# Performance work log

Hardware: AMD Instinct MI355X
Metric: run time of the kernel (lower is better)

Reference implementation:

```python
import jax, jax.numpy as jnp
import numpy as np

N, E = 50000, 400000
N_INP, H, D = 256, 4, 32
HID = H * D
TN, TE, L, N_OUT = 4, 6, 2, 16
SQRT_D = float(np.sqrt(D))


def setup_inputs() -> dict:
    key = jax.random.key(0)
    ks = jax.random.split(key, 16)
    s = 0.05
    return {
        "x": jax.random.normal(ks[0], (N, N_INP), jnp.float32),
        "adapt_W": jax.random.normal(ks[1], (TN, N_INP, HID), jnp.float32) * s,
        "adapt_b": jnp.zeros((TN, HID), jnp.float32),
        "Wk": jax.random.normal(ks[2], (L, TN, HID, HID), jnp.float32) * s,
        "Wq": jax.random.normal(ks[3], (L, TN, HID, HID), jnp.float32) * s,
        "Wv": jax.random.normal(ks[4], (L, TN, HID, HID), jnp.float32) * s,
        "pri": jnp.ones((L, H, TE), jnp.float32),
        "Wa": jax.random.normal(ks[5], (L, H, TE, D, D), jnp.float32) * s,
        "Wm": jax.random.normal(ks[6], (L, H, TE, D, D), jnp.float32) * s,
        "Wla": jax.random.normal(ks[7], (L, TN, HID, HID), jnp.float32) * s,
        "skip": jnp.ones((L, TN), jnp.float32),
        "gamma": jnp.ones((L, HID), jnp.float32),
        "beta": jnp.zeros((L, HID), jnp.float32),
        "out_W": jax.random.normal(ks[8], (HID, N_OUT), jnp.float32) * s,
        "out_b": jnp.zeros((N_OUT,), jnp.float32),
        "ntype": jax.random.randint(ks[9], (N,), 0, TN),
        "etype": jax.random.randint(ks[10], (E,), 0, TE),
        "src": jax.random.randint(ks[11], (E,), 0, N),
        "dst": jax.random.randint(ks[12], (E,), 0, N),
    }


def typed_linear(x, W, types):
    # out[i] = x[i] @ W[types[i]]  (TypedLinear / per-type nn.Linear loop)
    out = jnp.zeros((x.shape[0], W.shape[-1]), x.dtype)
    for t in range(W.shape[0]):
        out = jnp.where((types == t)[:, None], x @ W[t], out)
    return out


def hgt_layer(h, ntype, etype, src, dst, Wk, Wq, Wv, pri, Wa, Wm, Wla, skip, gamma, beta):
    k = typed_linear(h, Wk, ntype).reshape(N, H, D)
    q = typed_linear(h, Wq, ntype).reshape(N, H, D)
    v = typed_linear(h, Wv, ntype).reshape(N, H, D)
    k_e, q_e, v_e = k[src], q[dst], v[src]  # [E,H,D] gathers
    a = jnp.zeros((E, H), h.dtype)
    m = jnp.zeros((E, H, D), h.dtype)
    for t in range(TE):  # small fixed loop over edge types (relation matrices)
        sel = etype == t
        kw = jnp.einsum('ehd,hdo->eho', k_e, Wa[:, t])
        sc = (kw * q_e).sum(-1) * pri[:, t][None, :] / SQRT_D  # [E,H]
        a = jnp.where(sel[:, None], sc, a)
        mt = jnp.einsum('ehd,hdo->eho', v_e, Wm[:, t])
        m = jnp.where(sel[:, None, None], mt, m)
    # edge softmax over incoming edges of each destination node
    amax = jax.ops.segment_max(a, dst, num_segments=N)
    ex = jnp.exp(a - amax[dst])
    den = jax.ops.segment_sum(ex, dst, num_segments=N)
    attn = ex / den[dst]
    agg = jax.ops.segment_sum(m * attn[:, :, None], dst, num_segments=N).reshape(N, HID)
    ha = typed_linear(agg, Wla, ntype)
    alpha = jax.nn.sigmoid(skip)[ntype][:, None]
    out = ha * alpha + h * (1.0 - alpha)
    mu = out.mean(-1, keepdims=True)
    var = jnp.mean((out - mu) ** 2, -1, keepdims=True)
    return (out - mu) / jnp.sqrt(var + 1e-5) * gamma + beta


def forward(x, adapt_W, adapt_b, Wk, Wq, Wv, pri, Wa, Wm, Wla, skip, gamma, beta, out_W, out_b, ntype, etype, src, dst):
    # per-node-type adapt linear + exact GELU
    h = typed_linear(x, adapt_W, ntype) + adapt_b[ntype]
    h = jax.nn.gelu(h, approximate=False)
    for l in range(L):
        h = hgt_layer(h, ntype, etype, src, dst, Wk[l], Wq[l], Wv[l], pri[l], Wa[l], Wm[l], Wla[l], skip[l], gamma[l], beta[l])
    return h @ out_W + out_b


def reference(x, adapt_W, adapt_b, Wk, Wq, Wv, pri, Wa, Wm, Wla, skip, gamma, beta, out_W, out_b, ntype, etype, src, dst):
    return forward(x, adapt_W, adapt_b, Wk, Wq, Wv, pri, Wa, Wm, Wla, skip, gamma, beta, out_W, out_b, ntype, etype, src, dst)
```

## Files before the change

### kernel.cpp

```cpp
#include <hip/hip_runtime.h>
#include <hip/hip_bf16.h>
#include <math.h>

#define NN   50000
#define EE   400000
#define NINP 256
#define HH   4
#define DD   32
#define HIDD 128
#define TNN  4
#define TEE  6
#define LLL  2
#define NOUTT 16
#define NB   196


typedef __attribute__((ext_vector_type(8))) short bf16x8;
typedef __attribute__((ext_vector_type(4))) float f32x4;

__device__ __forceinline__ float bf_lo(unsigned u) { return __uint_as_float(u << 16); }
__device__ __forceinline__ float bf_hi(unsigned u) { return __uint_as_float(u & 0xFFFF0000u); }
__device__ __forceinline__ unsigned f2bf(float f) {
    unsigned u = __float_as_uint(f);
    u += 0x7FFFu + ((u >> 16) & 1u);
    return (u >> 16);
}

__global__ void k_init(int* __restrict__ deg, int* __restrict__ cur, int* __restrict__ ncnt,
                       int* __restrict__ ncur, int* __restrict__ nperm) {
    int i = blockIdx.x * 256 + threadIdx.x;
    if (i < NN) { deg[i] = 0; cur[i] = 0; }
    if (i < 16) { ncnt[i] = 0; ncur[i] = 0; }
    if (i < NN + 512) nperm[i] = -1;
}

__global__ void k_count_edges(const int* __restrict__ dst, int* __restrict__ deg) {
    int e = blockIdx.x * 256 + threadIdx.x;
    if (e < EE) atomicAdd(&deg[dst[e]], 1);
}
__global__ void k_count_types(const int* __restrict__ ntype, int* __restrict__ ncnt) {
    int n = blockIdx.x * 256 + threadIdx.x;
    int lane = threadIdx.x & 63;
    int t = (n < NN) ? ntype[n] : -1;
#pragma unroll
    for (int tt = 0; tt < TNN; tt++) {
        unsigned long long mask = __ballot(t == tt);
        if (mask && lane == (__ffsll((unsigned long long)mask) - 1))
            atomicAdd(&ncnt[tt], __popcll(mask));
    }
}
__global__ void k_scan1(const int* __restrict__ deg, int* __restrict__ bsum) {
    int i = blockIdx.x * 256 + threadIdx.x;
    int lane = threadIdx.x & 63, wv = threadIdx.x >> 6;
    __shared__ int ws[4];
    int x = (i < NN) ? deg[i] : 0;
#pragma unroll
    for (int off = 1; off < 64; off <<= 1) x += __shfl_xor(x, off);
    if (lane == 0) ws[wv] = x;
    __syncthreads();
    if (threadIdx.x == 0) bsum[blockIdx.x] = ws[0] + ws[1] + ws[2] + ws[3];
}
__global__ void k_scan2(const int* __restrict__ bsum, int* __restrict__ bpre,
                        const int* __restrict__ ncnt, int* __restrict__ meta) {
    __shared__ int ws[4];
    int tid = threadIdx.x, lane = tid & 63, wv = tid >> 6;
    int v = (tid < NB) ? bsum[tid] : 0;
    int x = v;
#pragma unroll
    for (int off = 1; off < 64; off <<= 1) {
        int y = __shfl_up(x, off);
        if (lane >= off) x += y;
    }
    if (lane == 63) ws[wv] = x;
    __syncthreads();
    if (tid == 0) { int a = 0; for (int w = 0; w < 4; w++) { int s = ws[w]; ws[w] = a; a += s; } }
    __syncthreads();
    if (tid < NB) bpre[tid] = x - v + ws[wv];
    if (tid == 0) {
        int acc = 0;
        meta[0] = 0;
        for (int t = 0; t < TNN; t++) { acc += ((ncnt[t] + 63) >> 6) << 6; meta[t + 1] = acc; }
    }
}
__global__ void k_scan3(const int* __restrict__ deg, const int* __restrict__ bpre,
                        int* __restrict__ offs) {
    int b = blockIdx.x;
    int tid = threadIdx.x, lane = tid & 63, wv = tid >> 6;
    int i = b * 256 + tid;
    __shared__ int ws[4];
    int v = (i < NN) ? deg[i] : 0;
    int x = v;
#pragma unroll
    for (int off = 1; off < 64; off <<= 1) {
        int y = __shfl_up(x, off);
        if (lane >= off) x += y;
    }
    if (lane == 63) ws[wv] = x;
    __syncthreads();
    if (tid == 0) { int a = 0; for (int w = 0; w < 4; w++) { int s = ws[w]; ws[w] = a; a += s; } }
    __syncthreads();
    if (i < NN) offs[i + 1] = x + ws[wv] + bpre[b];
    if (b == 0 && tid == 0) offs[0] = 0;
}
__global__ void k_scatter_edges(const int* __restrict__ dst, const int* __restrict__ offs,
                                int* __restrict__ cur, int* __restrict__ eidx) {
    int e = blockIdx.x * 256 + threadIdx.x;
    if (e < EE) {
        int d = dst[e];
        int p = atomicAdd(&cur[d], 1);
        eidx[offs[d] + p] = e;
    }
}
__global__ void k_scatter_nodes(const int* __restrict__ ntype, const int* __restrict__ meta,
                                int* __restrict__ ncur, int* __restrict__ nperm) {
    int n = blockIdx.x * 256 + threadIdx.x;
    int lane = threadIdx.x & 63;
    int t = (n < NN) ? ntype[n] : -1;
#pragma unroll
    for (int tt = 0; tt < TNN; tt++) {
        unsigned long long mask = __ballot(t == tt);
        if (t == tt) {
            int rank = __popcll(mask & ((1ull << lane) - 1ull));
            int leader = __ffsll((unsigned long long)mask) - 1;
            int b = 0;
            if (rank == 0) b = atomicAdd(&ncur[tt], __popcll(mask));
            b = __shfl(b, leader);
            nperm[meta[tt] + b + rank] = n;
        }
    }
}

__global__ void k_cvt_x(const float* __restrict__ x, unsigned short* __restrict__ xb) {
    size_t i = ((size_t)blockIdx.x * 256 + threadIdx.x) * 8;
    float4 a = *(const float4*)(x + i);
    float4 b = *(const float4*)(x + i + 4);
    uint4 pk;
    pk.x = f2bf(a.x) | (f2bf(a.y) << 16);
    pk.y = f2bf(a.z) | (f2bf(a.w) << 16);
    pk.z = f2bf(b.x) | (f2bf(b.y) << 16);
    pk.w = f2bf(b.z) | (f2bf(b.w) << 16);
    *(uint4*)(xb + i) = pk;
}

__global__ void k_wt(const float* __restrict__ adapt_W, const float* __restrict__ Wk,
                     const float* __restrict__ Wla, unsigned short* __restrict__ adaptT,
                     unsigned short* __restrict__ Wf, unsigned short* __restrict__ WlaT) {
    __shared__ float Ts[64][68];
    int b = blockIdx.x, tid = threadIdx.x;
    const float* src;
    unsigned short* dst;
    int K, kt, nt;
    if (b < 32) {
        int t = b >> 3, tile = b & 7;
        K = 256; kt = tile >> 1; nt = tile & 1;
        src = adapt_W + (size_t)t * 256 * 128;
        dst = adaptT + (size_t)t * 128 * 256;
    } else if (b < 64) {
        int b2 = b - 32, l = b2 >> 4, r = b2 & 15, t = r >> 2, tile = r & 3;
        K = 128; kt = tile >> 1; nt = tile & 1;
        src = Wk + (size_t)(l * 4 + t) * 16384;
        dst = Wf + (size_t)(l * TNN + t) * 1664 * 128;
    } else {
        int b2 = b - 64, l = b2 >> 4, r = b2 & 15, t = r >> 2, tile = r & 3;
        K = 128; kt = tile >> 1; nt = tile & 1;
        src = Wla + (size_t)(l * 4 + t) * 16384;
        dst = WlaT + (size_t)(l * 4 + t) * 16384;
    }
    int k0 = kt * 64, n0 = nt * 64;
#pragma unroll
    for (int it = 0; it < 4; it++) {
        int idx = tid + it * 256;
        int row = idx >> 4, c4 = (idx & 15) * 4;
        *(float4*)(&Ts[row][c4]) = *(const float4*)(src + (size_t)(k0 + row) * 128 + n0 + c4);
    }
    __syncthreads();
#pragma unroll
    for (int it = 0; it < 2; it++) {
        int idx = tid + it * 256;
        int nn = idx >> 3, sg = (idx & 7) * 8;
        uint4 pk;
        pk.x = f2bf(Ts[sg + 0][nn]) | (f2bf(Ts[sg + 1][nn]) << 16);
        pk.y = f2bf(Ts[sg + 2][nn]) | (f2bf(Ts[sg + 3][nn]) << 16);
        pk.z = f2bf(Ts[sg + 4][nn]) | (f2bf(Ts[sg + 5][nn]) << 16);
        pk.w = f2bf(Ts[sg + 6][nn]) | (f2bf(Ts[sg + 7][nn]) << 16);
        *(uint4*)(dst + (size_t)(n0 + nn) * K + k0 + sg) = pk;
    }
}

__global__ void k_comb(const float* __restrict__ Wq, const float* __restrict__ Wa,
                       const float* __restrict__ Wv, const float* __restrict__ Wm,
                       const float* __restrict__ pri, unsigned short* __restrict__ Wf) {
    __shared__ float Ls[128][36];
    __shared__ float Ss[32][36];
    __shared__ unsigned short Ot[32][136];
    int b = blockIdx.x, tid = threadIdx.x;
    int mode = b / 192;
    int rem = b % 192;
    int l = rem / 96;
    int rem2 = rem % 96;
    int t = rem2 / 24;
    int ht = rem2 % 24;
    int hh = ht / 6, te = ht % 6;
    const float* L = (mode == 0 ? Wq : Wv) + ((size_t)(l * TNN + t)) * 16384;
    const float* S = (mode == 0 ? Wa : Wm) + ((size_t)((l * HH + hh) * TEE + te)) * 1024;
    float ps = (mode == 0) ? pri[(l * HH + hh) * TEE + te] * 0.17677669529663687f : 1.0f;
#pragma unroll
    for (int it = 0; it < 4; it++) {
        int idx = tid + it * 256;
        int kk = idx >> 3, c4 = (idx & 7) * 4;
        *(float4*)(&Ls[kk][c4]) = *(const float4*)(L + (size_t)kk * 128 + hh * 32 + c4);
    }
    {
        int r = tid >> 3, c4 = (tid & 7) * 4;
        *(float4*)(&Ss[r][c4]) = *(const float4*)(S + r * 32 + c4);
    }
    __syncthreads();
    int k = tid >> 1, half = tid & 1;
#pragma unroll
    for (int jj = 0; jj < 16; jj++) {
        int j = half * 16 + jj;
        float s = 0.f;
        if (mode == 0) {
#pragma unroll
            for (int o = 0; o < 32; o++) s += Ls[k][o] * Ss[j][o];
        } else {
#pragma unroll
            for (int d = 0; d < 32; d++) s += Ls[k][d] * Ss[d][j];
        }
        Ot[j][k] = (unsigned short)f2bf(s * ps);
    }
    __syncthreads();
    unsigned short* dst = Wf + ((size_t)(l * TNN + t) * 1664 + (mode == 0 ? 128 : 896)) * 128;
#pragma unroll
    for (int it = 0; it < 2; it++) {
        int idx = tid + it * 256;
        int j = idx >> 4, sg = (idx & 15) * 8;
        uint4 pk = *(const uint4*)(&Ot[j][sg]);
        int jg = (hh * 6 + te) * 32 + j;
        *(uint4*)(dst + (size_t)jg * 128 + sg) = pk;
    }
}

template <int K, int NCB, int EPI, int OMODE>
__launch_bounds__(256) __global__
void k_gemm(const unsigned short* __restrict__ A, const unsigned short* __restrict__ WT,
            const float* __restrict__ bias, float* __restrict__ Yf,
            unsigned short* __restrict__ Yb, const int* __restrict__ nperm,
            const int* __restrict__ meta) {
    __shared__ __align__(16) char smem[52224];
    unsigned short* Ab = (unsigned short*)smem;
    unsigned short* Bs = (unsigned short*)(smem + 17408);
    float* Cb = (float*)(smem + 17408);
    const int WIDTH = NCB * 128;
    int row0 = blockIdx.x * 64;
    if (row0 >= meta[4]) return;
    int t = 0;
    while (t < 3 && row0 >= meta[t + 1]) t++;
    const unsigned short* WTt = WT + (size_t)t * WIDTH * K;
    int tid = threadIdx.x;
    int lane = tid & 63, w = tid >> 6;
    int m = lane & 15, q = lane >> 4;

#pragma unroll 1
    for (int cb = 0; cb < NCB; cb++) {
        f32x4 acc[8];
#pragma unroll
        for (int g = 0; g < 8; g++) acc[g] = (f32x4){0.f, 0.f, 0.f, 0.f};
#pragma unroll
        for (int kc = 0; kc < K / 128; kc++) {
            __syncthreads();
            if (NCB == 1 || cb == 0) {
#pragma unroll
                for (int it = 0; it < 4; it++) {
                    int idx = tid + it * 256;
                    int r = idx >> 4, sg = idx & 15;
                    int node = nperm[row0 + r];
                    uint4 v = make_uint4(0, 0, 0, 0);
                    if (node >= 0) v = *(const uint4*)(A + (size_t)node * K + kc * 128 + sg * 8);
                    *(uint4*)(Ab + r * 136 + sg * 8) = v;
                }
            }
#pragma unroll
            for (int it = 0; it < 8; it++) {
                int idx = tid + it * 256;
                int n = idx >> 4, sg = idx & 15;
                *(uint4*)(Bs + n * 136 + sg * 8) =
                    *(const uint4*)(WTt + (size_t)(cb * 128 + n) * K + kc * 128 + sg * 8);
            }
            __syncthreads();
#pragma unroll
            for (int k0 = 0; k0 < 128; k0 += 32) {
                bf16x8 a = *(const bf16x8*)(Ab + (w * 16 + m) * 136 + k0 + q * 8);
#pragma unroll
                for (int g = 0; g < 8; g++) {
                    bf16x8 bb = *(const bf16x8*)(Bs + (g * 16 + m) * 136 + k0 + q * 8);
                    acc[g] = __builtin_amdgcn_mfma_f32_16x16x32_bf16(a, bb, acc[g], 0, 0, 0);
                }
            }
        }
        __syncthreads();
#pragma unroll
        for (int g = 0; g < 8; g++)
#pragma unroll
            for (int r = 0; r < 4; r++)
                Cb[(w * 16 + q * 4 + r) * 132 + g * 16 + m] = acc[g][r];
        __syncthreads();
#pragma unroll
        for (int it = 0; it < 8; it++) {
            int idx = tid + it * 256;
            int row = idx >> 5, c4 = (idx & 31) * 4;
            int node = nperm[row0 + row];
            if (node < 0) continue;
            float4 v = *(const float4*)(Cb + row * 132 + c4);
            if (EPI == 1) {
                float4 bv = *(const float4*)(bias + t * 128 + c4);
                v.x += bv.x; v.y += bv.y; v.z += bv.z; v.w += bv.w;
                const float is2 = 0.70710678118654752f;
                v.x = 0.5f * v.x * (1.f + erff(v.x * is2));
                v.y = 0.5f * v.y * (1.f + erff(v.y * is2));
                v.z = 0.5f * v.z * (1.f + erff(v.z * is2));
                v.w = 0.5f * v.w * (1.f + erff(v.w * is2));
            }
            int col = cb * 128 + c4;
            if (OMODE == 0 || OMODE == 2)
                *(float4*)(Yf + (size_t)node * WIDTH + col) = v;
            if (OMODE == 1 || OMODE == 2) {
                uint2 pk;
                pk.x = f2bf(v.x) | (f2bf(v.y) << 16);
                pk.y = f2bf(v.z) | (f2bf(v.w) << 16);
                *(uint2*)(Yb + (size_t)node * WIDTH + col) = pk;
            }
        }
    }
}

__global__ void k_edge(const unsigned short* __restrict__ kqv,
                       const int* __restrict__ offs, const int* __restrict__ eidx,
                       const int* __restrict__ src, const int* __restrict__ etype,
                       unsigned short* __restrict__ aggb) {
    int lane = threadIdx.x & 63;
    int wid = blockIdx.x * (blockDim.x >> 6) + (threadIdx.x >> 6);
    int nw = gridDim.x * (blockDim.x >> 6);
    int h = lane >> 4;
    int i2 = (lane & 15) * 2;
    int hoff = h * 32 + i2;
    for (int n = wid; n < NN; n += nw) {
        int e0 = offs[n], e1 = offs[n + 1];
        float ax = 0.f, ay = 0.f, den = 0.f;
        const unsigned short* qrow = kqv + (size_t)n * 1664 + 128;
        int sA = 0, tA = 0, sB = 0, tB = 0;
        if (e0 < e1) { int e = eidx[e0]; sA = src[e]; tA = etype[e]; }
        if (e0 + 1 < e1) { int e = eidx[e0 + 1]; sB = src[e]; tB = etype[e]; }
        int j = e0;
        while (j + 1 < e1) {
            int toA = (h * 6 + tA) * 32 + i2;
            int toB = (h * 6 + tB) * 32 + i2;
            unsigned kuA = *(const unsigned*)(kqv + (size_t)sA * 1664 + hoff);
            unsigned quA = *(const unsigned*)(qrow + toA);
            unsigned vuA = *(const unsigned*)(kqv + (size_t)sA * 1664 + 896 + toA);
            unsigned kuB = *(const unsigned*)(kqv + (size_t)sB * 1664 + hoff);
            unsigned quB = *(const unsigned*)(qrow + toB);
            unsigned vuB = *(const unsigned*)(kqv + (size_t)sB * 1664 + 896 + toB);
            int jn = j + 2;
            if (jn < e1) { int e = eidx[jn]; sA = src[e]; tA = etype[e]; }
            if (jn + 1 < e1) { int e = eidx[jn + 1]; sB = src[e]; tB = etype[e]; }
            float pA = bf_lo(kuA) * bf_lo(quA) + bf_hi(kuA) * bf_hi(quA);
            float pB = bf_lo(kuB) * bf_lo(quB) + bf_hi(kuB) * bf_hi(quB);
            pA += __shfl_xor(pA, 1); pB += __shfl_xor(pB, 1);
            pA += __shfl_xor(pA, 2); pB += __shfl_xor(pB, 2);
            pA += __shfl_xor(pA, 4); pB += __shfl_xor(pB, 4);
            pA += __shfl_xor(pA, 8); pB += __shfl_xor(pB, 8);
            float exA = __expf(pA), exB = __expf(pB);
            den += exA + exB;
            ax += exA * bf_lo(vuA) + exB * bf_lo(vuB);
            ay += exA * bf_hi(vuA) + exB * bf_hi(vuB);
            j = jn;
        }
        if (j < e1) {
            int toA = (h * 6 + tA) * 32 + i2;
            unsigned kuA = *(const unsigned*)(kqv + (size_t)sA * 1664 + hoff);
            unsigned quA = *(const unsigned*)(qrow + toA);
            unsigned vuA = *(const unsigned*)(kqv + (size_t)sA * 1664 + 896 + toA);
            float pA = bf_lo(kuA) * bf_lo(quA) + bf_hi(kuA) * bf_hi(quA);
            pA += __shfl_xor(pA, 1);
            pA += __shfl_xor(pA, 2);
            pA += __shfl_xor(pA, 4);
            pA += __shfl_xor(pA, 8);
            float exA = __expf(pA);
            den += exA;
            ax += exA * bf_lo(vuA);
            ay += exA * bf_hi(vuA);
        }
        float r = (den > 0.f) ? (1.0f / den) : 0.f;
        unsigned pk = f2bf(ax * r) | (f2bf(ay * r) << 16);
        *(unsigned*)(aggb + (size_t)n * 128 + hoff) = pk;
    }
}

__global__ void k_blend_ln(const float* __restrict__ ha, float* __restrict__ h,
                           unsigned short* __restrict__ hb, const int* __restrict__ ntype,
                           const float* __restrict__ skip, const float* __restrict__ gamma,
                           const float* __restrict__ beta) {
    int lane = threadIdx.x & 63;
    int w = threadIdx.x >> 6;
    int n = blockIdx.x * 4 + w;
    if (n >= NN) return;
    int off = lane * 2;
    int t = ntype[n];
    float alpha = 1.0f / (1.0f + __expf(-skip[t]));
    float2 a2 = *(const float2*)(ha + (size_t)n * 128 + off);
    float2 h2 = *(const float2*)(h + (size_t)n * 128 + off);
    float ox = a2.x * alpha + h2.x * (1.f - alpha);
    float oy = a2.y * alpha + h2.y * (1.f - alpha);
    float s = ox + oy;
#pragma unroll
    for (int m = 1; m < 64; m <<= 1) s += __shfl_xor(s, m);
    float mu = s * (1.0f / 128.0f);
    float dx = ox - mu, dy = oy - mu;
    float v = dx * dx + dy * dy;
#pragma unroll
    for (int m = 1; m < 64; m <<= 1) v += __shfl_xor(v, m);
    float rs = rsqrtf(v * (1.0f / 128.0f) + 1e-5f);
    float2 g2 = *(const float2*)(gamma + off);
    float2 b2 = *(const float2*)(beta + off);
    float vx = dx * rs * g2.x + b2.x;
    float vy = dy * rs * g2.y + b2.y;
    *(float2*)(h + (size_t)n * 128 + off) = make_float2(vx, vy);
    *(unsigned*)(hb + (size_t)n * 128 + off) = f2bf(vx) | (f2bf(vy) << 16);
}

__global__ void k_out(const float* __restrict__ h, const float* __restrict__ Wo,
                      const float* __restrict__ bo, float* __restrict__ out) {
    __shared__ float Ws[128 * 16];
    int tid = threadIdx.x;
#pragma unroll
    for (int it = 0; it < 2; it++) {
        int idx = (tid + it * 256) * 4;
        *(float4*)(&Ws[idx]) = *(const float4*)(Wo + idx);
    }
    __syncthreads();
    int nl = tid >> 4;
    int o = tid & 15;
    int n = blockIdx.x * 16 + nl;
    float acc = bo[o];
    const float* hr = h + (size_t)n * 128;
#pragma unroll
    for (int kk = 0; kk < 128; kk += 4) {
        float4 hv = *(const float4*)(hr + kk);
        acc += hv.x * Ws[kk * 16 + o] + hv.y * Ws[(kk + 1) * 16 + o] +
               hv.z * Ws[(kk + 2) * 16 + o] + hv.w * Ws[(kk + 3) * 16 + o];
    }
    out[(size_t)n * 16 + o] = acc;
}

extern "C" void kernel_launch(void* const* d_in, const int* in_sizes, int n_in,
                              void* d_out, int out_size, void* d_ws, size_t ws_size,
                              hipStream_t stream) {
    const float* x       = (const float*)d_in[0];
    const float* adapt_W = (const float*)d_in[1];
    const float* adapt_b = (const float*)d_in[2];
    const float* Wk      = (const float*)d_in[3];
    const float* Wq      = (const float*)d_in[4];
    const float* Wv      = (const float*)d_in[5];
    const float* pri     = (const float*)d_in[6];
    const float* Wa      = (const float*)d_in[7];
    const float* Wm      = (const float*)d_in[8];
    const float* Wla     = (const float*)d_in[9];
    const float* skip    = (const float*)d_in[10];
    const float* gamma   = (const float*)d_in[11];
    const float* beta    = (const float*)d_in[12];
    const float* out_W   = (const float*)d_in[13];
    const float* out_b   = (const float*)d_in[14];
    const int* ntype     = (const int*)d_in[15];
    const int* etype     = (const int*)d_in[16];
    const int* src       = (const int*)d_in[17];
    const int* dst       = (const int*)d_in[18];
    float* out = (float*)d_out;

    char* p = (char*)d_ws;
    auto al = [](size_t v) { return (v + 255) & ~(size_t)255; };
    float* h  = (float*)p;          p += al((size_t)NN * 128 * 4);
    float* ha = (float*)p;          p += al((size_t)NN * 128 * 4);
    unsigned short* xb = (unsigned short*)ha;
    unsigned short* hb   = (unsigned short*)p; p += al((size_t)NN * 128 * 2);
    unsigned short* aggb = (unsigned short*)p; p += al((size_t)NN * 128 * 2);
    unsigned short* kqvb = (unsigned short*)p; p += al((size_t)NN * 1664 * 2);
    unsigned short* adaptT = (unsigned short*)p; p += al((size_t)TNN * 128 * 256 * 2);
    unsigned short* WlaT   = (unsigned short*)p; p += al((size_t)LLL * TNN * 16384 * 2);
    unsigned short* Wf     = (unsigned short*)p; p += al((size_t)LLL * TNN * 1664 * 128 * 2);
    int* deg   = (int*)p; p += al((size_t)NN * 4);
    int* offs  = (int*)p; p += al((size_t)(NN + 1) * 4);
    int* cur   = (int*)p; p += al((size_t)NN * 4);
    int* eidx  = (int*)p; p += al((size_t)EE * 4);
    int* nperm = (int*)p; p += al((size_t)(NN + 512) * 4);
    int* bsum  = (int*)p; p += al(256 * 4);
    int* bpre  = (int*)p; p += al(256 * 4);
    int* ncnt  = (int*)p; p += al(64);
    int* ncur  = (int*)p; p += al(64);
    int* meta  = (int*)p; p += al(64);

    k_init<<<(NN + 512 + 255) / 256, 256, 0, stream>>>(deg, cur, ncnt, ncur, nperm);
    k_count_edges<<<(EE + 255) / 256, 256, 0, stream>>>(dst, deg);
    k_count_types<<<(NN + 255) / 256, 256, 0, stream>>>(ntype, ncnt);
    k_scan1<<<NB, 256, 0, stream>>>(deg, bsum);
    k_scan2<<<1, 256, 0, stream>>>(bsum, bpre, ncnt, meta);
    k_scan3<<<NB, 256, 0, stream>>>(deg, bpre, offs);
    k_scatter_edges<<<(EE + 255) / 256, 256, 0, stream>>>(dst, offs, cur, eidx);
    k_scatter_nodes<<<(NN + 255) / 256, 256, 0, stream>>>(ntype, meta, ncur, nperm);

    k_cvt_x<<<(NN * 256 / 8 + 255) / 256, 256, 0, stream>>>(x, xb);
    k_wt<<<96, 256, 0, stream>>>(adapt_W, Wk, Wla, adaptT, Wf, WlaT);
    k_comb<<<384, 256, 0, stream>>>(Wq, Wa, Wv, Wm, pri, Wf);

    const int TILES = NN / 64 + TNN + 1;

    k_gemm<256, 1, 1, 2><<<TILES, 256, 0, stream>>>(xb, adaptT, adapt_b, h, hb, nperm, meta);

    for (int l = 0; l < LLL; l++) {
        k_gemm<128, 13, 0, 1><<<TILES, 256, 0, stream>>>(
            hb, Wf + (size_t)l * TNN * 1664 * 128, nullptr, nullptr, kqvb, nperm, meta);

        k_edge<<<4096, 256, 0, stream>>>(kqvb, offs, eidx, src, etype, aggb);

        k_gemm<128, 1, 0, 0><<<TILES, 256, 0, stream>>>(
            aggb, WlaT + (size_t)l * TNN * 16384, nullptr, ha, nullptr, nperm, meta);
        k_blend_ln<<<(NN + 3) / 4, 256, 0, stream>>>(ha, h, hb, ntype, skip + (size_t)l * TNN,
                                                     gamma + (size_t)l * HIDD,
                                                     beta + (size_t)l * HIDD);
    }

    k_out<<<NN / 16, 256, 0, stream>>>(h, out_W, out_b, out);
}
```

Before: 668.2 us.

## Fuse x conversion into GEMM load, blend+LayerNorm into GEMM epilogue, widen edge unroll

The fp32→bf16 conversion of x now happens while the adapt GEMM loads its A tile, so the separate conversion kernel and its intermediate buffer go away. The skip blend and LayerNorm are folded into the Wla GEMM epilogue, which removes the ha round trip and the separate k_blend_ln launch. The edge attention loop is unrolled to four edges per iteration to put more gathers in flight. The output projection now reads the bf16 copy of h, which trades some precision for half the read traffic. The fused epilogue runs the LayerNorm rows serially per wave, which may lower its parallelism.

```diff
diff --git a/kernel.cpp b/kernel.cpp
--- a/kernel.cpp
+++ b/kernel.cpp
@@ -128,18 +128,6 @@
             nperm[meta[tt] + b + rank] = n;
         }
     }
-}
-
-__global__ void k_cvt_x(const float* __restrict__ x, unsigned short* __restrict__ xb) {
-    size_t i = ((size_t)blockIdx.x * 256 + threadIdx.x) * 8;
-    float4 a = *(const float4*)(x + i);
-    float4 b = *(const float4*)(x + i + 4);
-    uint4 pk;
-    pk.x = f2bf(a.x) | (f2bf(a.y) << 16);
-    pk.y = f2bf(a.z) | (f2bf(a.w) << 16);
-    pk.z = f2bf(b.x) | (f2bf(b.y) << 16);
-    pk.w = f2bf(b.z) | (f2bf(b.w) << 16);
-    *(uint4*)(xb + i) = pk;
 }
 
 __global__ void k_wt(const float* __restrict__ adapt_W, const float* __restrict__ Wk,
@@ -241,12 +229,14 @@
     }
 }
 
-template <int K, int NCB, int EPI, int OMODE>
+template <int K, int NCB, int EPI, int OMODE, int AF32>
 __launch_bounds__(256) __global__
-void k_gemm(const unsigned short* __restrict__ A, const unsigned short* __restrict__ WT,
+void k_gemm(const void* __restrict__ Av, const unsigned short* __restrict__ WT,
             const float* __restrict__ bias, float* __restrict__ Yf,
             unsigned short* __restrict__ Yb, const int* __restrict__ nperm,
-            const int* __restrict__ meta) {
+            const int* __restrict__ meta, const float* __restrict__ skipv,
+            const float* __restrict__ gamma, const float* __restrict__ beta,
+            float* __restrict__ hres, unsigned short* __restrict__ hbout) {
     __shared__ __align__(16) char smem[52224];
     unsigned short* Ab = (unsigned short*)smem;
     unsigned short* Bs = (unsigned short*)(smem + 17408);
@@ -270,14 +260,33 @@
         for (int kc = 0; kc < K / 128; kc++) {
             __syncthreads();
             if (NCB == 1 || cb == 0) {
-#pragma unroll
-                for (int it = 0; it < 4; it++) {
-                    int idx = tid + it * 256;
-                    int r = idx >> 4, sg = idx & 15;
-                    int node = nperm[row0 + r];
-                    uint4 v = make_uint4(0, 0, 0, 0);
-                    if (node >= 0) v = *(const uint4*)(A + (size_t)node * K + kc * 128 + sg * 8);
-                    *(uint4*)(Ab + r * 136 + sg * 8) = v;
+                if (AF32) {
+                    const float* A = (const float*)Av;
+#pragma unroll
+                    for (int it = 0; it < 8; it++) {
+                        int idx = tid + it * 256;
+                        int r = idx >> 5, c4 = (idx & 31) * 4;
+                        int node = nperm[row0 + r];
+                        float4 v = make_float4(0.f, 0.f, 0.f, 0.f);
+                        if (node >= 0)
+                            v = *(const float4*)(A + (size_t)node * K + kc * 128 + c4);
+                        uint2 pk;
+                        pk.x = f2bf(v.x) | (f2bf(v.y) << 16);
+                        pk.y = f2bf(v.z) | (f2bf(v.w) << 16);
+                        *(uint2*)(Ab + r * 136 + c4) = pk;
+                    }
+                } else {
+                    const unsigned short* A = (const unsigned short*)Av;
+#pragma unroll
+                    for (int it = 0; it < 4; it++) {
+                        int idx = tid + it * 256;
+                        int r = idx >> 4, sg = idx & 15;
+                        int node = nperm[row0 + r];
+                        uint4 v = make_uint4(0, 0, 0, 0);
+                        if (node >= 0)
+                            v = *(const uint4*)(A + (size_t)node * K + kc * 128 + sg * 8);
+                        *(uint4*)(Ab + r * 136 + sg * 8) = v;
+                    }
                 }
             }
 #pragma unroll
@@ -305,30 +314,61 @@
             for (int r = 0; r < 4; r++)
                 Cb[(w * 16 + q * 4 + r) * 132 + g * 16 + m] = acc[g][r];
         __syncthreads();
-#pragma unroll
-        for (int it = 0; it < 8; it++) {
-            int idx = tid + it * 256;
-            int row = idx >> 5, c4 = (idx & 31) * 4;
-            int node = nperm[row0 + row];
-            if (node < 0) continue;
-            float4 v = *(const float4*)(Cb + row * 132 + c4);
-            if (EPI == 1) {
-                float4 bv = *(const float4*)(bias + t * 128 + c4);
-                v.x += bv.x; v.y += bv.y; v.z += bv.z; v.w += bv.w;
-                const float is2 = 0.70710678118654752f;
-                v.x = 0.5f * v.x * (1.f + erff(v.x * is2));
-                v.y = 0.5f * v.y * (1.f + erff(v.y * is2));
-                v.z = 0.5f * v.z * (1.f + erff(v.z * is2));
-                v.w = 0.5f * v.w * (1.f + erff(v.w * is2));
-            }
-            int col = cb * 128 + c4;
-            if (OMODE == 0 || OMODE == 2)
-                *(float4*)(Yf + (size_t)node * WIDTH + col) = v;
-            if (OMODE == 1 || OMODE == 2) {
-                uint2 pk;
-                pk.x = f2bf(v.x) | (f2bf(v.y) << 16);
-                pk.y = f2bf(v.z) | (f2bf(v.w) << 16);
-                *(uint2*)(Yb + (size_t)node * WIDTH + col) = pk;
+        if (EPI == 2) {
+            float alpha = 1.0f / (1.0f + __expf(-skipv[t]));
+            int off = lane * 2;
+            float2 g2 = *(const float2*)(gamma + off);
+            float2 b2 = *(const float2*)(beta + off);
+#pragma unroll 1
+            for (int it = 0; it < 16; it++) {
+                int row = w * 16 + it;
+                int node = nperm[row0 + row];
+                if (node < 0) continue;
+                float ax = Cb[row * 132 + off];
+                float ay = Cb[row * 132 + off + 1];
+                float2 h2 = *(const float2*)(hres + (size_t)node * 128 + off);
+                float ox = ax * alpha + h2.x * (1.f - alpha);
+                float oy = ay * alpha + h2.y * (1.f - alpha);
+                float s = ox + oy;
+#pragma unroll
+                for (int mm = 1; mm < 64; mm <<= 1) s += __shfl_xor(s, mm);
+                float mu = s * (1.0f / 128.0f);
+                float dx = ox - mu, dy = oy - mu;
+                float v2 = dx * dx + dy * dy;
+#pragma unroll
+                for (int mm = 1; mm < 64; mm <<= 1) v2 += __shfl_xor(v2, mm);
+                float rs = rsqrtf(v2 * (1.0f / 128.0f) + 1e-5f);
+                float vx = dx * rs * g2.x + b2.x;
+                float vy = dy * rs * g2.y + b2.y;
+                *(float2*)(hres + (size_t)node * 128 + off) = make_float2(vx, vy);
+                *(unsigned*)(hbout + (size_t)node * 128 + off) = f2bf(vx) | (f2bf(vy) << 16);
+            }
+        } else {
+#pragma unroll
+            for (int it = 0; it < 8; it++) {
+                int idx = tid + it * 256;
+                int row = idx >> 5, c4 = (idx & 31) * 4;
+                int node = nperm[row0 + row];
+                if (node < 0) continue;
+                float4 v = *(const float4*)(Cb + row * 132 + c4);
+                if (EPI == 1) {
+                    float4 bv = *(const float4*)(bias + t * 128 + c4);
+                    v.x += bv.x; v.y += bv.y; v.z += bv.z; v.w += bv.w;
+                    const float is2 = 0.70710678118654752f;
+                    v.x = 0.5f * v.x * (1.f + erff(v.x * is2));
+                    v.y = 0.5f * v.y * (1.f + erff(v.y * is2));
+                    v.z = 0.5f * v.z * (1.f + erff(v.z * is2));
+                    v.w = 0.5f * v.w * (1.f + erff(v.w * is2));
+                }
+                int col = cb * 128 + c4;
+                if (OMODE == 0 || OMODE == 2)
+                    *(float4*)(Yf + (size_t)node * WIDTH + col) = v;
+                if (OMODE == 1 || OMODE == 2) {
+                    uint2 pk;
+                    pk.x = f2bf(v.x) | (f2bf(v.y) << 16);
+                    pk.y = f2bf(v.z) | (f2bf(v.w) << 16);
+                    *(uint2*)(Yb + (size_t)node * WIDTH + col) = pk;
+                }
             }
         }
     }
@@ -348,48 +388,58 @@
         int e0 = offs[n], e1 = offs[n + 1];
         float ax = 0.f, ay = 0.f, den = 0.f;
         const unsigned short* qrow = kqv + (size_t)n * 1664 + 128;
-        int sA = 0, tA = 0, sB = 0, tB = 0;
-        if (e0 < e1) { int e = eidx[e0]; sA = src[e]; tA = etype[e]; }
-        if (e0 + 1 < e1) { int e = eidx[e0 + 1]; sB = src[e]; tB = etype[e]; }
+        int s[4], t[4];
+#pragma unroll
+        for (int u = 0; u < 4; u++) {
+            s[u] = 0; t[u] = 0;
+            if (e0 + u < e1) { int e = eidx[e0 + u]; s[u] = src[e]; t[u] = etype[e]; }
+        }
         int j = e0;
-        while (j + 1 < e1) {
-            int toA = (h * 6 + tA) * 32 + i2;
-            int toB = (h * 6 + tB) * 32 + i2;
-            unsigned kuA = *(const unsigned*)(kqv + (size_t)sA * 1664 + hoff);
-            unsigned quA = *(const unsigned*)(qrow + toA);
-            unsigned vuA = *(const unsigned*)(kqv + (size_t)sA * 1664 + 896 + toA);
-            unsigned kuB = *(const unsigned*)(kqv + (size_t)sB * 1664 + hoff);
-            unsigned quB = *(const unsigned*)(qrow + toB);
-            unsigned vuB = *(const unsigned*)(kqv + (size_t)sB * 1664 + 896 + toB);
-            int jn = j + 2;
-            if (jn < e1) { int e = eidx[jn]; sA = src[e]; tA = etype[e]; }
-            if (jn + 1 < e1) { int e = eidx[jn + 1]; sB = src[e]; tB = etype[e]; }
-            float pA = bf_lo(kuA) * bf_lo(quA) + bf_hi(kuA) * bf_hi(quA);
-            float pB = bf_lo(kuB) * bf_lo(quB) + bf_hi(kuB) * bf_hi(quB);
-            pA += __shfl_xor(pA, 1); pB += __shfl_xor(pB, 1);
-            pA += __shfl_xor(pA, 2); pB += __shfl_xor(pB, 2);
-            pA += __shfl_xor(pA, 4); pB += __shfl_xor(pB, 4);
-            pA += __shfl_xor(pA, 8); pB += __shfl_xor(pB, 8);
-            float exA = __expf(pA), exB = __expf(pB);
-            den += exA + exB;
-            ax += exA * bf_lo(vuA) + exB * bf_lo(vuB);
-            ay += exA * bf_hi(vuA) + exB * bf_hi(vuB);
+        while (j + 3 < e1) {
+            unsigned ku[4], qu[4], vu[4];
+#pragma unroll
+            for (int u = 0; u < 4; u++) {
+                int to = (h * 6 + t[u]) * 32 + i2;
+                ku[u] = *(const unsigned*)(kqv + (size_t)s[u] * 1664 + hoff);
+                qu[u] = *(const unsigned*)(qrow + to);
+                vu[u] = *(const unsigned*)(kqv + (size_t)s[u] * 1664 + 896 + to);
+            }
+            int jn = j + 4;
+#pragma unroll
+            for (int u = 0; u < 4; u++)
+                if (jn + u < e1) { int e = eidx[jn + u]; s[u] = src[e]; t[u] = etype[e]; }
+            float p[4];
+#pragma unroll
+            for (int u = 0; u < 4; u++)
+                p[u] = bf_lo(ku[u]) * bf_lo(qu[u]) + bf_hi(ku[u]) * bf_hi(qu[u]);
+#pragma unroll
+            for (int mm = 1; mm < 16; mm <<= 1) {
+#pragma unroll
+                for (int u = 0; u < 4; u++) p[u] += __shfl_xor(p[u], mm);
+            }
+#pragma unroll
+            for (int u = 0; u < 4; u++) {
+                float ex = __expf(p[u]);
+                den += ex;
+                ax += ex * bf_lo(vu[u]);
+                ay += ex * bf_hi(vu[u]);
+            }
             j = jn;
         }
-        if (j < e1) {
-            int toA = (h * 6 + tA) * 32 + i2;
-            unsigned kuA = *(const unsigned*)(kqv + (size_t)sA * 1664 + hoff);
-            unsigned quA = *(const unsigned*)(qrow + toA);
-            unsigned vuA = *(const unsigned*)(kqv + (size_t)sA * 1664 + 896 + toA);
-            float pA = bf_lo(kuA) * bf_lo(quA) + bf_hi(kuA) * bf_hi(quA);
-            pA += __shfl_xor(pA, 1);
-            pA += __shfl_xor(pA, 2);
-            pA += __shfl_xor(pA, 4);
-            pA += __shfl_xor(pA, 8);
-            float exA = __expf(pA);
-            den += exA;
-            ax += exA * bf_lo(vuA);
-            ay += exA * bf_hi(vuA);
+        for (int u = 0; j < e1; j++, u++) {
+            int to = (h * 6 + t[u]) * 32 + i2;
+            unsigned ku = *(const unsigned*)(kqv + (size_t)s[u] * 1664 + hoff);
+            unsigned qu = *(const unsigned*)(qrow + to);
+            unsigned vu = *(const unsigned*)(kqv + (size_t)s[u] * 1664 + 896 + to);
+            float p0 = bf_lo(ku) * bf_lo(qu) + bf_hi(ku) * bf_hi(qu);
+            p0 += __shfl_xor(p0, 1);
+            p0 += __shfl_xor(p0, 2);
+            p0 += __shfl_xor(p0, 4);
+            p0 += __shfl_xor(p0, 8);
+            float ex = __expf(p0);
+            den += ex;
+            ax += ex * bf_lo(vu);
+            ay += ex * bf_hi(vu);
         }
         float r = (den > 0.f) ? (1.0f / den) : 0.f;
         unsigned pk = f2bf(ax * r) | (f2bf(ay * r) << 16);
@@ -397,39 +447,7 @@
     }
 }
 
-__global__ void k_blend_ln(const float* __restrict__ ha, float* __restrict__ h,
-                           unsigned short* __restrict__ hb, const int* __restrict__ ntype,
-                           const float* __restrict__ skip, const float* __restrict__ gamma,
-                           const float* __restrict__ beta) {
-    int lane = threadIdx.x & 63;
-    int w = threadIdx.x >> 6;
-    int n = blockIdx.x * 4 + w;
-    if (n >= NN) return;
-    int off = lane * 2;
-    int t = ntype[n];
-    float alpha = 1.0f / (1.0f + __expf(-skip[t]));
-    float2 a2 = *(const float2*)(ha + (size_t)n * 128 + off);
-    float2 h2 = *(const float2*)(h + (size_t)n * 128 + off);
-    float ox = a2.x * alpha + h2.x * (1.f - alpha);
-    float oy = a2.y * alpha + h2.y * (1.f - alpha);
-    float s = ox + oy;
-#pragma unroll
-    for (int m = 1; m < 64; m <<= 1) s += __shfl_xor(s, m);
-    float mu = s * (1.0f / 128.0f);
-    float dx = ox - mu, dy = oy - mu;
-    float v = dx * dx + dy * dy;
-#pragma unroll
-    for (int m = 1; m < 64; m <<= 1) v += __shfl_xor(v, m);
-    float rs = rsqrtf(v * (1.0f / 128.0f) + 1e-5f);
-    float2 g2 = *(const float2*)(gamma + off);
-    float2 b2 = *(const float2*)(beta + off);
-    float vx = dx * rs * g2.x + b2.x;
-    float vy = dy * rs * g2.y + b2.y;
-    *(float2*)(h + (size_t)n * 128 + off) = make_float2(vx, vy);
-    *(unsigned*)(hb + (size_t)n * 128 + off) = f2bf(vx) | (f2bf(vy) << 16);
-}
-
-__global__ void k_out(const float* __restrict__ h, const float* __restrict__ Wo,
+__global__ void k_out(const unsigned short* __restrict__ hb, const float* __restrict__ Wo,
                       const float* __restrict__ bo, float* __restrict__ out) {
     __shared__ float Ws[128 * 16];
     int tid = threadIdx.x;
@@ -443,12 +461,14 @@
     int o = tid & 15;
     int n = blockIdx.x * 16 + nl;
     float acc = bo[o];
-    const float* hr = h + (size_t)n * 128;
-#pragma unroll
-    for (int kk = 0; kk < 128; kk += 4) {
-        float4 hv = *(const float4*)(hr + kk);
-        acc += hv.x * Ws[kk * 16 + o] + hv.y * Ws[(kk + 1) * 16 + o] +
-               hv.z * Ws[(kk + 2) * 16 + o] + hv.w * Ws[(kk + 3) * 16 + o];
+    const unsigned short* hr = hb + (size_t)n * 128;
+#pragma unroll
+    for (int kk = 0; kk < 128; kk += 8) {
+        uint4 hv = *(const uint4*)(hr + kk);
+        acc += bf_lo(hv.x) * Ws[(kk + 0) * 16 + o] + bf_hi(hv.x) * Ws[(kk + 1) * 16 + o] +
+               bf_lo(hv.y) * Ws[(kk + 2) * 16 + o] + bf_hi(hv.y) * Ws[(kk + 3) * 16 + o] +
+               bf_lo(hv.z) * Ws[(kk + 4) * 16 + o] + bf_hi(hv.z) * Ws[(kk + 5) * 16 + o] +
+               bf_lo(hv.w) * Ws[(kk + 6) * 16 + o] + bf_hi(hv.w) * Ws[(kk + 7) * 16 + o];
     }
     out[(size_t)n * 16 + o] = acc;
 }
@@ -480,8 +500,6 @@
     char* p = (char*)d_ws;
     auto al = [](size_t v) { return (v + 255) & ~(size_t)255; };
     float* h  = (float*)p;          p += al((size_t)NN * 128 * 4);
-    float* ha = (float*)p;          p += al((size_t)NN * 128 * 4);
-    unsigned short* xb = (unsigned short*)ha;
     unsigned short* hb   = (unsigned short*)p; p += al((size_t)NN * 128 * 2);
     unsigned short* aggb = (unsigned short*)p; p += al((size_t)NN * 128 * 2);
     unsigned short* kqvb = (unsigned short*)p; p += al((size_t)NN * 1664 * 2);
@@ -508,26 +526,26 @@
     k_scatter_edges<<<(EE + 255) / 256, 256, 0, stream>>>(dst, offs, cur, eidx);
     k_scatter_nodes<<<(NN + 255) / 256, 256, 0, stream>>>(ntype, meta, ncur, nperm);
 
-    k_cvt_x<<<(NN * 256 / 8 + 255) / 256, 256, 0, stream>>>(x, xb);
     k_wt<<<96, 256, 0, stream>>>(adapt_W, Wk, Wla, adaptT, Wf, WlaT);
     k_comb<<<384, 256, 0, stream>>>(Wq, Wa, Wv, Wm, pri, Wf);
 
     const int TILES = NN / 64 + TNN + 1;
 
-    k_gemm<256, 1, 1, 2><<<TILES, 256, 0, stream>>>(xb, adaptT, adapt_b, h, hb, nperm, meta);
+    k_gemm<256, 1, 1, 2, 1><<<TILES, 256, 0, stream>>>(
+        x, adaptT, adapt_b, h, hb, nperm, meta, nullptr, nullptr, nullptr, nullptr, nullptr);
 
     for (int l = 0; l < LLL; l++) {
-        k_gemm<128, 13, 0, 1><<<TILES, 256, 0, stream>>>(
-            hb, Wf + (size_t)l * TNN * 1664 * 128, nullptr, nullptr, kqvb, nperm, meta);
+        k_gemm<128, 13, 0, 1, 0><<<TILES, 256, 0, stream>>>(
+            hb, Wf + (size_t)l * TNN * 1664 * 128, nullptr, nullptr, kqvb, nperm, meta,
+            nullptr, nullptr, nullptr, nullptr, nullptr);
 
         k_edge<<<4096, 256, 0, stream>>>(kqvb, offs, eidx, src, etype, aggb);
 
-        k_gemm<128, 1, 0, 0><<<TILES, 256, 0, stream>>>(
-            aggb, WlaT + (size_t)l * TNN * 16384, nullptr, ha, nullptr, nperm, meta);
-        k_blend_ln<<<(NN + 3) / 4, 256, 0, stream>>>(ha, h, hb, ntype, skip + (size_t)l * TNN,
-                                                     gamma + (size_t)l * HIDD,
-                                                     beta + (size_t)l * HIDD);
-    }
-
-    k_out<<<NN / 16, 256, 0, stream>>>(h, out_W, out_b, out);
-}
+        k_gemm<128, 1, 2, 0, 0><<<TILES, 256, 0, stream>>>(
+            aggb, WlaT + (size_t)l * TNN * 16384, nullptr, nullptr, nullptr, nperm, meta,
+            skip + (size_t)l * TNN, gamma + (size_t)l * HIDD, beta + (size_t)l * HIDD,
+            h, hb);
+    }
+
+    k_out<<<NN / 16, 256, 0, stream>>>(hb, out_W, out_b, out);
+}
```

Measured after the change: 681.7 us. +2.0%, slower.
